# Kernel optimization log

Measured on AMD Instinct MI355X. Metric: run time of the kernel, lower is better.

Reference implementation:

```python
import jax, jax.numpy as jnp
import numpy as np

NUM_CATS = 5
EPS = 1e-6


def setup_inputs() -> dict:
    key = jax.random.key(0)
    k1, k2, k3, k4 = jax.random.split(key, 4)
    B, C, H, W = 64, 3, 256, 256
    restored = jax.random.normal(k1, (B, C, H, W), dtype=jnp.float32)
    clean_patch_1 = jax.random.normal(k2, (B, C, H, W), dtype=jnp.float32)
    un = jax.random.uniform(k3, (B, C, H, W), dtype=jnp.float32)
    de_id = jax.random.randint(k4, (B,), 0, NUM_CATS)
    return {"restored": restored, "clean_patch_1": clean_patch_1,
            "de_id": de_id, "un": un}


def _loss(restored, clean, un, de_id):
    B, C, H, W = restored.shape
    E = C * H * W  # elements per sample
    dt = restored.dtype

    onehot = (de_id[:, None] == jnp.arange(NUM_CATS)[None, :])  # [B,5] bool
    m = onehot.astype(dt)                                        # [B,5]
    counts = onehot.sum(0)                                       # [5] int
    nonempty = counts > 0
    safe_counts = jnp.maximum(counts, 1).astype(dt)              # avoid 0-div

    # Per-category mean uncertainty map: un_map[c] = mean_{i: de_id[i]=c} un[i] + eps
    un_sum = jnp.einsum('bk,bchw->kchw', m, un)                  # [5,C,H,W]
    un_map = un_sum / safe_counts[:, None, None, None] + EPS     # [5,C,H,W]
    s = 1.0 / un_map                                             # [5,C,H,W]

    # Per-sample scaled L1 (s gathered by each sample's category)
    absdiff = jnp.abs(clean - restored)                          # [B,C,H,W]
    scaled_sum_per_sample = (absdiff * s[de_id]).sum(axis=(1, 2, 3))  # [B]
    abs_sum_per_sample = absdiff.sum(axis=(1, 2, 3))                  # [B]

    cat_scaled_sum = jnp.einsum('bk,b->k', m, scaled_sum_per_sample)  # [5]
    cat_abs_sum = jnp.einsum('bk,b->k', m, abs_sum_per_sample)        # [5]

    # NOTE: the original code never clears un_hq_list/un_lq_list between
    # categories, so the L1 at category c is the mean over ALL samples from
    # categories 0..c (each scaled by its OWN category's s). Replicate that
    # via cumulative sums/counts over the category axis.
    cum_scaled = jnp.cumsum(cat_scaled_sum)                      # [5]
    cum_elems = jnp.cumsum(counts).astype(dt) * E                # [5]
    cum_l1 = cum_scaled / jnp.maximum(cum_elems, 1.0)            # [5]

    old_loss = jnp.where(nonempty, cat_abs_sum / (safe_counts * E), 0.0)
    un_num = un_map.mean(axis=(1, 2, 3))                         # [5]
    bn = jnp.where(nonempty, 2.0 * jnp.log(un_num), 0.0)
    unc_l1 = jnp.where(nonempty, cum_l1, 0.0)

    cat_losses = unc_l1 + bn                                     # [5]
    num = nonempty.sum().astype(dt)
    total = cat_losses.sum() / num
    return total, cat_losses, old_loss, bn, unc_l1


def reference(restored, clean_patch_1, de_id, un):
    return _loss(restored, clean_patch_1, un, de_id)
```

## Files before the change

kernel.cpp:

```cpp
#include <hip/hip_runtime.h>
#include <math.h>

#define NCAT  5
#define BATCH 64
#define ELEMS 196608
#define EPSV  1e-6f

__global__ __launch_bounds__(256) void accum_kernel(
    const float* __restrict__ restored,
    const float* __restrict__ clean,
    const int*   __restrict__ de_id,
    const float* __restrict__ un,
    float*       __restrict__ acc)
{
    __shared__ int   sh_de[BATCH];
    __shared__ float sred[4][3 * NCAT];

    const int tid = threadIdx.x;
    if (tid < BATCH) sh_de[tid] = de_id[tid];
    __syncthreads();

    int cnt[NCAT] = {0, 0, 0, 0, 0};
    #pragma unroll 8
    for (int b = 0; b < BATCH; ++b) {
        int k = sh_de[b];
        #pragma unroll
        for (int j = 0; j < NCAT; ++j) cnt[j] += (k == j) ? 1 : 0;
    }

    const int p = blockIdx.x * 256 + tid;
    float un_s[NCAT] = {0.f, 0.f, 0.f, 0.f, 0.f};
    float ad_s[NCAT] = {0.f, 0.f, 0.f, 0.f, 0.f};

    const float* rp = restored + p;
    const float* cp = clean + p;
    const float* up = un + p;

    #pragma unroll 4
    for (int b = 0; b < BATCH; ++b) {
        const long off = (long)b * ELEMS;
        float u  = up[off];
        float ad = fabsf(cp[off] - rp[off]);
        int   k  = sh_de[b];
        #pragma unroll
        for (int j = 0; j < NCAT; ++j) {
            float m = (k == j) ? 1.0f : 0.0f;
            un_s[j] = fmaf(m, u,  un_s[j]);
            ad_s[j] = fmaf(m, ad, ad_s[j]);
        }
    }

    float vals[3 * NCAT];
    #pragma unroll
    for (int j = 0; j < NCAT; ++j) {
        float safe   = (float)(cnt[j] > 0 ? cnt[j] : 1);
        float un_map = un_s[j] / safe + EPSV;
        vals[j]            = ad_s[j] / un_map;
        vals[NCAT + j]     = ad_s[j];
        vals[2 * NCAT + j] = un_s[j];
    }

    #pragma unroll
    for (int i = 0; i < 3 * NCAT; ++i) {
        float v = vals[i];
        #pragma unroll
        for (int off = 32; off >= 1; off >>= 1)
            v += __shfl_down(v, off, 64);
        vals[i] = v;
    }

    const int wave = tid >> 6;
    const int lane = tid & 63;
    if (lane == 0) {
        #pragma unroll
        for (int i = 0; i < 3 * NCAT; ++i) sred[wave][i] = vals[i];
    }
    __syncthreads();

    if (tid < 3 * NCAT) {
        float v = sred[0][tid] + sred[1][tid] + sred[2][tid] + sred[3][tid];
        atomicAdd(&acc[tid], v);
    }
}

__global__ void epilogue_kernel(const int*   __restrict__ de_id,
                                const float* __restrict__ acc,
                                float*       __restrict__ out)
{
    if (threadIdx.x != 0 || blockIdx.x != 0) return;

    int cnt[NCAT] = {0, 0, 0, 0, 0};
    for (int b = 0; b < BATCH; ++b) cnt[de_id[b]]++;

    const float Ef = (float)ELEMS;
    float cum_s = 0.f;
    long  cum_c = 0;
    float total = 0.f;
    int   num   = 0;

    float cat_losses[NCAT], old_loss[NCAT], bn[NCAT], unc_l1[NCAT];

    for (int j = 0; j < NCAT; ++j) {
        cum_s += acc[j];
        cum_c += cnt[j];
        float cum_elems = (float)cum_c * Ef;
        float cum_l1    = cum_s / fmaxf(cum_elems, 1.0f);

        bool  ne   = cnt[j] > 0;
        float safe = (float)(ne ? cnt[j] : 1);

        old_loss[j]  = ne ? acc[NCAT + j] / (safe * Ef) : 0.f;
        float un_num = acc[2 * NCAT + j] / (safe * Ef) + EPSV;
        bn[j]        = ne ? 2.0f * logf(un_num) : 0.f;
        unc_l1[j]    = ne ? cum_l1 : 0.f;
        cat_losses[j] = unc_l1[j] + bn[j];
        total += cat_losses[j];
        num   += ne ? 1 : 0;
    }
    total /= (float)num;

    out[0] = total;
    for (int j = 0; j < NCAT; ++j) {
        out[1 + j]  = cat_losses[j];
        out[6 + j]  = old_loss[j];
        out[11 + j] = bn[j];
        out[16 + j] = unc_l1[j];
    }
}

extern "C" void kernel_launch(void* const* d_in, const int* in_sizes, int n_in,
                              void* d_out, int out_size, void* d_ws, size_t ws_size,
                              hipStream_t stream) {
    (void)in_sizes; (void)n_in; (void)out_size; (void)ws_size;
    const float* restored = (const float*)d_in[0];
    const float* clean    = (const float*)d_in[1];
    const int*   de_id    = (const int*)d_in[2];
    const float* un       = (const float*)d_in[3];
    float* out = (float*)d_out;
    float* acc = (float*)d_ws;

    hipMemsetAsync(acc, 0, 3 * NCAT * sizeof(float), stream);
    accum_kernel<<<ELEMS / 256, 256, 0, stream>>>(restored, clean, de_id, un, acc);
    epilogue_kernel<<<1, 64, 0, stream>>>(de_id, acc, out);
}
```

Baseline: 177.4 us.

## Vectorize loads to float2, drop atomics and memset, parallelize epilogue reduction

```diff
diff --git a/kernel.cpp b/kernel.cpp
--- a/kernel.cpp
+++ b/kernel.cpp
@@ -4,60 +4,81 @@
 #define NCAT  5
 #define BATCH 64
 #define ELEMS 196608
-#define EPSV  1e-6f
+#define HALF_ELEMS 98304
+#define NBLK 768
+#define TPB  128
+#define EPSV 1e-6f
 
-__global__ __launch_bounds__(256) void accum_kernel(
-    const float* __restrict__ restored,
-    const float* __restrict__ clean,
-    const int*   __restrict__ de_id,
-    const float* __restrict__ un,
-    float*       __restrict__ acc)
+__global__ __launch_bounds__(TPB) void accum_kernel(
+    const float2* __restrict__ restored,
+    const float2* __restrict__ clean,
+    const int*    __restrict__ de_id,
+    const float2* __restrict__ un,
+    float*        __restrict__ partials)
 {
     __shared__ int   sh_de[BATCH];
-    __shared__ float sred[4][3 * NCAT];
+    __shared__ float sh_inv[NCAT];
+    __shared__ float sred[TPB / 64][3 * NCAT];
 
     const int tid = threadIdx.x;
-    if (tid < BATCH) sh_de[tid] = de_id[tid];
+
+    if (tid < 64) {
+        int k = de_id[tid];
+        sh_de[tid] = k;
+        #pragma unroll
+        for (int j = 0; j < NCAT; ++j) {
+            unsigned long long m = __ballot(k == j);
+            if (tid == j) {
+                int c = __popcll(m);
+                sh_inv[j] = 1.0f / (float)(c > 0 ? c : 1);
+            }
+        }
+    }
     __syncthreads();
 
-    int cnt[NCAT] = {0, 0, 0, 0, 0};
+    float inv_safe[NCAT];
+    #pragma unroll
+    for (int j = 0; j < NCAT; ++j) inv_safe[j] = sh_inv[j];
+
+    const int gid = blockIdx.x * TPB + tid;
+    const float2* rp = restored + gid;
+    const float2* cp = clean + gid;
+    const float2* up = un + gid;
+
+    float2 un_s[NCAT], ad_s[NCAT];
+    #pragma unroll
+    for (int j = 0; j < NCAT; ++j) {
+        un_s[j].x = un_s[j].y = 0.f;
+        ad_s[j].x = ad_s[j].y = 0.f;
+    }
+
     #pragma unroll 8
     for (int b = 0; b < BATCH; ++b) {
+        const size_t off = (size_t)b * HALF_ELEMS;
+        float2 u = up[off];
+        float2 c = cp[off];
+        float2 r = rp[off];
+        float adx = fabsf(c.x - r.x);
+        float ady = fabsf(c.y - r.y);
         int k = sh_de[b];
-        #pragma unroll
-        for (int j = 0; j < NCAT; ++j) cnt[j] += (k == j) ? 1 : 0;
-    }
-
-    const int p = blockIdx.x * 256 + tid;
-    float un_s[NCAT] = {0.f, 0.f, 0.f, 0.f, 0.f};
-    float ad_s[NCAT] = {0.f, 0.f, 0.f, 0.f, 0.f};
-
-    const float* rp = restored + p;
-    const float* cp = clean + p;
-    const float* up = un + p;
-
-    #pragma unroll 4
-    for (int b = 0; b < BATCH; ++b) {
-        const long off = (long)b * ELEMS;
-        float u  = up[off];
-        float ad = fabsf(cp[off] - rp[off]);
-        int   k  = sh_de[b];
         #pragma unroll
         for (int j = 0; j < NCAT; ++j) {
             float m = (k == j) ? 1.0f : 0.0f;
-            un_s[j] = fmaf(m, u,  un_s[j]);
-            ad_s[j] = fmaf(m, ad, ad_s[j]);
+            un_s[j].x = fmaf(m, u.x, un_s[j].x);
+            un_s[j].y = fmaf(m, u.y, un_s[j].y);
+            ad_s[j].x = fmaf(m, adx, ad_s[j].x);
+            ad_s[j].y = fmaf(m, ady, ad_s[j].y);
         }
     }
 
     float vals[3 * NCAT];
     #pragma unroll
     for (int j = 0; j < NCAT; ++j) {
-        float safe   = (float)(cnt[j] > 0 ? cnt[j] : 1);
-        float un_map = un_s[j] / safe + EPSV;
-        vals[j]            = ad_s[j] / un_map;
-        vals[NCAT + j]     = ad_s[j];
-        vals[2 * NCAT + j] = un_s[j];
+        float umx = fmaf(un_s[j].x, inv_safe[j], EPSV);
+        float umy = fmaf(un_s[j].y, inv_safe[j], EPSV);
+        vals[j]            = ad_s[j].x / umx + ad_s[j].y / umy;
+        vals[NCAT + j]     = ad_s[j].x + ad_s[j].y;
+        vals[2 * NCAT + j] = un_s[j].x + un_s[j].y;
     }
 
     #pragma unroll
@@ -78,53 +99,80 @@
     __syncthreads();
 
     if (tid < 3 * NCAT) {
-        float v = sred[0][tid] + sred[1][tid] + sred[2][tid] + sred[3][tid];
-        atomicAdd(&acc[tid], v);
+        float v = sred[0][tid] + sred[1][tid];
+        partials[tid * NBLK + blockIdx.x] = v;
     }
 }
 
-__global__ void epilogue_kernel(const int*   __restrict__ de_id,
-                                const float* __restrict__ acc,
-                                float*       __restrict__ out)
+__global__ __launch_bounds__(256) void epilogue_kernel(
+    const int*   __restrict__ de_id,
+    const float* __restrict__ partials,
+    float*       __restrict__ out)
 {
-    if (threadIdx.x != 0 || blockIdx.x != 0) return;
+    __shared__ int   sh_cnt[NCAT];
+    __shared__ float sh_acc[3 * NCAT];
 
-    int cnt[NCAT] = {0, 0, 0, 0, 0};
-    for (int b = 0; b < BATCH; ++b) cnt[de_id[b]]++;
+    const int tid = threadIdx.x;
 
-    const float Ef = (float)ELEMS;
-    float cum_s = 0.f;
-    long  cum_c = 0;
-    float total = 0.f;
-    int   num   = 0;
+    if (tid < 64) {
+        int k = de_id[tid];
+        #pragma unroll
+        for (int j = 0; j < NCAT; ++j) {
+            unsigned long long m = __ballot(k == j);
+            if (tid == j) sh_cnt[j] = __popcll(m);
+        }
+    }
 
-    float cat_losses[NCAT], old_loss[NCAT], bn[NCAT], unc_l1[NCAT];
+    if (tid < 240) {
+        const int row    = tid >> 4;
+        const int lane16 = tid & 15;
+        float v = 0.f;
+        #pragma unroll 4
+        for (int k = 0; k < NBLK / 16; ++k)
+            v += partials[row * NBLK + lane16 + (k << 4)];
+        v += __shfl_down(v, 8, 16);
+        v += __shfl_down(v, 4, 16);
+        v += __shfl_down(v, 2, 16);
+        v += __shfl_down(v, 1, 16);
+        if (lane16 == 0) sh_acc[row] = v;
+    }
+    __syncthreads();
 
-    for (int j = 0; j < NCAT; ++j) {
-        cum_s += acc[j];
-        cum_c += cnt[j];
-        float cum_elems = (float)cum_c * Ef;
-        float cum_l1    = cum_s / fmaxf(cum_elems, 1.0f);
+    if (tid == 0) {
+        const float Ef = (float)ELEMS;
+        float cum_s = 0.f;
+        long  cum_c = 0;
+        float total = 0.f;
+        int   num   = 0;
 
-        bool  ne   = cnt[j] > 0;
-        float safe = (float)(ne ? cnt[j] : 1);
+        float cat_losses[NCAT], old_loss[NCAT], bn[NCAT], unc_l1[NCAT];
 
-        old_loss[j]  = ne ? acc[NCAT + j] / (safe * Ef) : 0.f;
-        float un_num = acc[2 * NCAT + j] / (safe * Ef) + EPSV;
-        bn[j]        = ne ? 2.0f * logf(un_num) : 0.f;
-        unc_l1[j]    = ne ? cum_l1 : 0.f;
-        cat_losses[j] = unc_l1[j] + bn[j];
-        total += cat_losses[j];
-        num   += ne ? 1 : 0;
-    }
-    total /= (float)num;
+        for (int j = 0; j < NCAT; ++j) {
+            cum_s += sh_acc[j];
+            cum_c += sh_cnt[j];
+            float cum_elems = (float)cum_c * Ef;
+            float cum_l1    = cum_s / fmaxf(cum_elems, 1.0f);
 
-    out[0] = total;
-    for (int j = 0; j < NCAT; ++j) {
-        out[1 + j]  = cat_losses[j];
-        out[6 + j]  = old_loss[j];
-        out[11 + j] = bn[j];
-        out[16 + j] = unc_l1[j];
+            bool  ne   = sh_cnt[j] > 0;
+            float safe = (float)(ne ? sh_cnt[j] : 1);
+
+            old_loss[j]  = ne ? sh_acc[NCAT + j] / (safe * Ef) : 0.f;
+            float un_num = sh_acc[2 * NCAT + j] / (safe * Ef) + EPSV;
+            bn[j]        = ne ? 2.0f * logf(un_num) : 0.f;
+            unc_l1[j]    = ne ? cum_l1 : 0.f;
+            cat_losses[j] = unc_l1[j] + bn[j];
+            total += cat_losses[j];
+            num   += ne ? 1 : 0;
+        }
+        total /= (float)num;
+
+        out[0] = total;
+        for (int j = 0; j < NCAT; ++j) {
+            out[1 + j]  = cat_losses[j];
+            out[6 + j]  = old_loss[j];
+            out[11 + j] = bn[j];
+            out[16 + j] = unc_l1[j];
+        }
     }
 }
 
@@ -132,14 +180,13 @@
                               void* d_out, int out_size, void* d_ws, size_t ws_size,
                               hipStream_t stream) {
     (void)in_sizes; (void)n_in; (void)out_size; (void)ws_size;
-    const float* restored = (const float*)d_in[0];
-    const float* clean    = (const float*)d_in[1];
-    const int*   de_id    = (const int*)d_in[2];
-    const float* un       = (const float*)d_in[3];
-    float* out = (float*)d_out;
-    float* acc = (float*)d_ws;
+    const float2* restored = (const float2*)d_in[0];
+    const float2* clean    = (const float2*)d_in[1];
+    const int*    de_id    = (const int*)d_in[2];
+    const float2* un       = (const float2*)d_in[3];
+    float* out      = (float*)d_out;
+    float* partials = (float*)d_ws;
 
-    hipMemsetAsync(acc, 0, 3 * NCAT * sizeof(float), stream);
-    accum_kernel<<<ELEMS / 256, 256, 0, stream>>>(restored, clean, de_id, un, acc);
-    epilogue_kernel<<<1, 64, 0, stream>>>(de_id, acc, out);
+    accum_kernel<<<NBLK, TPB, 0, stream>>>(restored, clean, de_id, un, partials);
+    epilogue_kernel<<<1, 256, 0, stream>>>(de_id, partials, out);
 }
```

Measured after the change: 176.2 us. No clear change (-0.6%).
